# Optimization experiments

Measured on AMD Instinct MI355X. Metric: run time of the kernel, lower is better.

## Reference

```python
import jax, jax.numpy as jnp
from jax import lax
import numpy as np

D = 56      # latent_rep_size
H = 501     # GRU hidden size
T = 277     # repeat length (sequence length)
O = 76      # fc2 output


def setup_inputs() -> dict:
    key = jax.random.key(0)
    ks = jax.random.split(key, 20)
    B = 256
    s = 0.05
    inp = {"x": jax.random.normal(ks[0], (B, D), dtype=jnp.float32)}
    inp["fc1_w"] = jax.random.normal(ks[1], (D, D), dtype=jnp.float32) * s
    inp["fc1_b"] = jax.random.normal(ks[2], (D,), dtype=jnp.float32) * s
    k = 3
    for l, in_dim in enumerate([D, H, H]):
        inp[f"w_ih{l}"] = jax.random.normal(ks[k], (3 * H, in_dim), dtype=jnp.float32) * s; k += 1
        inp[f"w_hh{l}"] = jax.random.normal(ks[k], (3 * H, H), dtype=jnp.float32) * s; k += 1
        inp[f"b_ih{l}"] = jax.random.normal(ks[k], (3 * H,), dtype=jnp.float32) * s; k += 1
        inp[f"b_hh{l}"] = jax.random.normal(ks[k], (3 * H,), dtype=jnp.float32) * s; k += 1
    inp["fc2_w"] = jax.random.normal(ks[k], (O, H), dtype=jnp.float32) * s; k += 1
    inp["fc2_b"] = jax.random.normal(ks[k], (O,), dtype=jnp.float32) * s
    return inp


def _gru_step(h, g, w_hh, b_hh):
    # g: precomputed input gates (B, 3H) in PyTorch order [r, z, n]
    hg = h @ w_hh.T + b_hh                       # (B, 3H)
    r = jax.nn.sigmoid(g[:, :H] + hg[:, :H])
    z = jax.nn.sigmoid(g[:, H:2 * H] + hg[:, H:2 * H])
    n = jnp.tanh(g[:, 2 * H:] + r * hg[:, 2 * H:])
    h_new = (1.0 - z) * n + z * h
    return h_new, h_new


def _gru_layer(x_gates, w_hh, b_hh, B, dtype):
    # x_gates: (T, B, 3H) input contribution per timestep
    h0 = jnp.zeros((B, H), dtype)
    _, ys = lax.scan(lambda h, g: _gru_step(h, g, w_hh, b_hh), h0, x_gates)
    return ys  # (T, B, H)


def reference(x, fc1_w, fc1_b,
              w_ih0, w_hh0, b_ih0, b_hh0,
              w_ih1, w_hh1, b_ih1, b_hh1,
              w_ih2, w_hh2, b_ih2, b_hh2,
              fc2_w, fc2_b):
    B = x.shape[0]
    dtype = x.dtype
    # fc1 + relu, then the input is repeated 277 times -> layer-0 input gates
    # are identical at every timestep; compute them once (B, 3H).
    h_in = jax.nn.relu(x @ fc1_w.T + fc1_b)             # (B, D)
    g0 = h_in @ w_ih0.T + b_ih0                          # (B, 3H), constant over t
    h0 = jnp.zeros((B, H), dtype)
    _, ys0 = lax.scan(lambda h, _: _gru_step(h, g0, w_hh0, b_hh0), h0, None, length=T)
    # layers 1 and 2: precompute input gates for all timesteps, then scan
    g1 = jnp.einsum('tbh,gh->tbg', ys0, w_ih1) + b_ih1   # (T, B, 3H)
    ys1 = _gru_layer(g1, w_hh1, b_hh1, B, dtype)
    g2 = jnp.einsum('tbh,gh->tbg', ys1, w_ih2) + b_ih2
    ys2 = _gru_layer(g2, w_hh2, b_hh2, B, dtype)
    # fc2 then permute(1, 2, 0): (T, B, O) -> (B, O, T)
    out = jnp.einsum('tbh,oh->tbo', ys2, fc2_w) + fc2_b
    return jnp.transpose(out, (1, 2, 0))
```

## Files before the change

### kernel.cpp

```cpp
#include <hip/hip_runtime.h>
#include <hip/hip_bf16.h>
#include <math.h>

#define D_IN 56
#define H    501
#define T_STEPS 277
#define O_OUT 76
#define BATCH 256
#define HP   512
#define NP   1504
#define SSTR 520
#define HSTR 576

#define LDS_SA    0
#define LDS_SB    (32 * SSTR)
#define LDS_SC    (64 * SSTR)
#define LDS_STAGE (96 * SSTR)
#define DYN_LDS   (96 * SSTR * 2 + 18 * HSTR * 4 + 32 * 48 * 4 + 3 * 4 * 16 * 4)

typedef __attribute__((ext_vector_type(8))) short s16x8;
typedef __attribute__((ext_vector_type(4))) float f32x4;
typedef unsigned long long ull;

__device__ __forceinline__ short f2bf(float x) {
    union { float f; unsigned u; } v; v.f = x;
    unsigned r = (v.u + 0x7fffu + ((v.u >> 16) & 1u)) >> 16;
    return (short)r;
}
__device__ __forceinline__ float bf2f(short b) {
    union { unsigned u; float f; } v; v.u = ((unsigned)(unsigned short)b) << 16;
    return v.f;
}
__device__ __forceinline__ float sigm(float x) { return 1.f / (1.f + __expf(-x)); }
__device__ __forceinline__ float tanh_fast(float x) { return 1.f - 2.f / (1.f + __expf(2.f * x)); }

__device__ __forceinline__ void glds16(const void* g, void* l) {
    __builtin_amdgcn_global_load_lds((const __attribute__((address_space(1))) unsigned int*)g,
                                     (__attribute__((address_space(3))) unsigned int*)l,
                                     16, 0, 0);
}

__global__ void k_pack_gru(const float* __restrict__ w_ih,
                           const float* __restrict__ w_hh,
                           short* __restrict__ dst, int KT) {
    int tile = blockIdx.x;
    int ktp  = tile % KT;
    int g    = (tile / KT) % 3;
    int j    = tile / (KT * 3);
    int l    = threadIdx.x;
    int u    = j * 16 + (l & 15);
    int row  = g * H + u;
    const float* src; int k0;
    if (KT == 32) {
        if (ktp < 16) { src = w_ih; k0 = ktp * 32; }
        else          { src = w_hh; k0 = (ktp - 16) * 32; }
    } else          { src = w_hh; k0 = ktp * 32; }
    k0 += (l >> 4) * 8;
    short* p = dst + ((size_t)tile * 64 + l) * 8;
    for (int jj = 0; jj < 8; jj++) {
        int k = k0 + jj;
        float v = 0.f;
        if (u < H && k < H) v = src[(size_t)row * H + k];
        p[jj] = f2bf(v);
    }
}

__global__ void k_pack_fc2(const float* __restrict__ w, short* __restrict__ dst) {
    int tile = blockIdx.x;
    int kt = tile % 16, mt = tile / 16;
    int l = threadIdx.x;
    int o = mt * 16 + (l & 15);
    int k0 = kt * 32 + (l >> 4) * 8;
    short* p = dst + ((size_t)tile * 64 + l) * 8;
    for (int jj = 0; jj < 8; jj++) {
        int k = k0 + jj; float v = 0.f;
        if (o < O_OUT && k < H) v = w[(size_t)o * H + k];
        p[jj] = f2bf(v);
    }
}

__global__ void k_hin(const float* __restrict__ x, const float* __restrict__ w,
                      const float* __restrict__ bias, float* __restrict__ hin) {
    int b = blockIdx.x, o = threadIdx.x;
    float acc = 0.f;
    if (o < D_IN) {
        acc = bias[o];
        for (int k = 0; k < D_IN; k++) acc += x[b * D_IN + k] * w[o * D_IN + k];
        acc = fmaxf(acc, 0.f);
    }
    hin[b * 64 + o] = (o < D_IN) ? acc : 0.f;
}

__global__ void k_g0(const float* __restrict__ hin, const float* __restrict__ w_ih0,
                     const float* __restrict__ b_ih0, float* __restrict__ g0) {
    int b = blockIdx.x, tid = threadIdx.x;
    __shared__ float shx[D_IN];
    if (tid < D_IN) shx[tid] = hin[b * 64 + tid];
    __syncthreads();
    for (int o = tid; o < NP; o += 256) {
        float acc = 0.f;
        if (o < 3 * H) {
            acc = b_ih0[o];
            for (int k = 0; k < D_IN; k++) acc += shx[k] * w_ih0[(size_t)o * D_IN + k];
        }
        g0[(size_t)b * NP + o] = acc;
    }
}

template <int NK>
__device__ __forceinline__ void role_mfma_reg(const short* __restrict__ stg, int abase, int ak0,
                                              const s16x8 (&wv)[48],
                                              float* __restrict__ dr, float* __restrict__ dz,
                                              float* __restrict__ dn, int lane) {
    const int arow = lane & 15;
    const int acol = (lane >> 4) * 8;
    f32x4 ar0 = {0.f,0.f,0.f,0.f}, ar1 = {0.f,0.f,0.f,0.f};
    f32x4 az0 = {0.f,0.f,0.f,0.f}, az1 = {0.f,0.f,0.f,0.f};
    f32x4 an0 = {0.f,0.f,0.f,0.f}, an1 = {0.f,0.f,0.f,0.f};
    #pragma unroll
    for (int kk = 0; kk < NK; kk++) {
        int ak = ak0 + kk;
        s16x8 x0 = *(const s16x8*)&stg[abase + arow * SSTR + ak * 32 + acol];
        s16x8 x1 = *(const s16x8*)&stg[abase + (16 + arow) * SSTR + ak * 32 + acol];
        ar0 = __builtin_amdgcn_mfma_f32_16x16x32_bf16(x0, wv[3 * kk + 0], ar0, 0, 0, 0);
        ar1 = __builtin_amdgcn_mfma_f32_16x16x32_bf16(x1, wv[3 * kk + 0], ar1, 0, 0, 0);
        az0 = __builtin_amdgcn_mfma_f32_16x16x32_bf16(x0, wv[3 * kk + 1], az0, 0, 0, 0);
        az1 = __builtin_amdgcn_mfma_f32_16x16x32_bf16(x1, wv[3 * kk + 1], az1, 0, 0, 0);
        an0 = __builtin_amdgcn_mfma_f32_16x16x32_bf16(x0, wv[3 * kk + 2], an0, 0, 0, 0);
        an1 = __builtin_amdgcn_mfma_f32_16x16x32_bf16(x1, wv[3 * kk + 2], an1, 0, 0, 0);
    }
    int ul = lane & 15, mrow = (lane >> 4) * 4;
    #pragma unroll
    for (int r = 0; r < 4; r++) {
        dr[(mrow + r) * 18 + ul]      = ar0[r];
        dr[(16 + mrow + r) * 18 + ul] = ar1[r];
        dz[(mrow + r) * 18 + ul]      = az0[r];
        dz[(16 + mrow + r) * 18 + ul] = az1[r];
        dn[(mrow + r) * 18 + ul]      = an0[r];
        dn[(16 + mrow + r) * 18 + ul] = an1[r];
    }
}

__global__ __launch_bounds__(384, 2)
void k_gru_persist(const short* __restrict__ packW0,
                   const short* __restrict__ packW1,
                   const short* __restrict__ packW2,
                   const float* __restrict__ g0,
                   const float* __restrict__ b_hh0,
                   const float* __restrict__ b_ih1, const float* __restrict__ b_hh1,
                   const float* __restrict__ b_ih2, const float* __restrict__ b_hh2,
                   short* __restrict__ ysA,
                   short* __restrict__ ysB,
                   unsigned* __restrict__ cnt) {
    const int bg   = blockIdx.x & 7;
    const int j    = blockIdx.x >> 3;
    const int b0   = bg * 32;
    const int tid  = threadIdx.x;
    const int lane = tid & 63;
    const int wave = tid >> 6;
    const s16x8 z8 = {0, 0, 0, 0, 0, 0, 0, 0};

    extern __shared__ __align__(16) char smem[];
    short* stg = (short*)smem;
    float* hgl = (float*)(smem + LDS_STAGE * 2);
    float* sg0 = hgl + 18 * HSTR;
    float* sbb = sg0 + 32 * 48;

    int abase, ak0, slot0;
    s16x8 wv[48];
    {
        const short* wpk; int KT, kt0;
        switch (wave) {
            case 0:  wpk = packW0; KT = 16; kt0 = 0;  abase = LDS_SA; ak0 = 0; slot0 = 0;  break;
            case 1:  wpk = packW0; KT = 16; kt0 = 8;  abase = LDS_SA; ak0 = 8; slot0 = 1;  break;
            case 2:  wpk = packW1; KT = 32; kt0 = 0;  abase = LDS_SA; ak0 = 0; slot0 = 6;  break;
            case 3:  wpk = packW1; KT = 32; kt0 = 16; abase = LDS_SB; ak0 = 0; slot0 = 7;  break;
            case 4:  wpk = packW2; KT = 32; kt0 = 0;  abase = LDS_SB; ak0 = 0; slot0 = 12; break;
            default: wpk = packW2; KT = 32; kt0 = 16; abase = LDS_SC; ak0 = 0; slot0 = 13; break;
        }
        const volatile s16x8* vg0 = (const volatile s16x8*)(wpk + ((size_t)((j * 3 + 0) * KT + kt0) * 512));
        const volatile s16x8* vg1 = (const volatile s16x8*)(wpk + ((size_t)((j * 3 + 1) * KT + kt0) * 512));
        const volatile s16x8* vg2 = (const volatile s16x8*)(wpk + ((size_t)((j * 3 + 2) * KT + kt0) * 512));
        const int NKw = (wave < 2) ? 8 : 16;
        #pragma unroll
        for (int kk = 0; kk < 16; kk++) {
            if (kk < NKw) {
                wv[3 * kk + 0] = vg0[kk * 64 + lane];
                wv[3 * kk + 1] = vg1[kk * 64 + lane];
                wv[3 * kk + 2] = vg2[kk * 64 + lane];
            }
        }
    }
    float* dr = hgl + (size_t)slot0 * HSTR;
    float* dz = hgl + (size_t)(slot0 + 2) * HSTR;
    float* dn = hgl + (size_t)(slot0 + 4) * HSTR;

    for (int c = tid; c < 32 * 48; c += 384) {
        int m = c / 48, col = c % 48;
        int g = col >> 4, ul = col & 15;
        int u = j * 16 + ul;
        float v = 0.f;
        if (u < H) {
            v = g0[(size_t)(b0 + m) * NP + g * H + u];
            if (g == 0) v += b_hh0[u];
            else if (g == 1) v += b_hh0[H + u];
        }
        sg0[m * 48 + col] = v;
    }
    if (tid < 48) {
        int l = tid >> 4, ul = tid & 15, u = j * 16 + ul;
        float br = 0.f, bz = 0.f, bxn = 0.f, bhn = 0.f;
        if (u < H) {
            if (l == 0) bhn = b_hh0[2 * H + u];
            else {
                const float* bi = (l == 1) ? b_ih1 : b_ih2;
                const float* bh = (l == 1) ? b_hh1 : b_hh2;
                br = bi[u] + bh[u]; bz = bi[H + u] + bh[H + u];
                bxn = bi[2 * H + u]; bhn = bh[2 * H + u];
            }
        }
        sbb[(l * 4 + 0) * 16 + ul] = br;  sbb[(l * 4 + 1) * 16 + ul] = bz;
        sbb[(l * 4 + 2) * 16 + ul] = bxn; sbb[(l * 4 + 3) * 16 + ul] = bhn;
    }
    __syncthreads();

    unsigned* myflags = cnt + bg * 32;

    for (int s = 0; s < T_STEPS + 2; ++s) {
        const bool hasL0 = (s < T_STEPS);
        const bool hasL1 = (s >= 1 && s <= T_STEPS);
        const bool hasL2 = (s >= 2);
        const short* ysAm1 = ysA + (size_t)(s - 1) * BATCH * HP;
        const short* ysBm2 = ysB + (size_t)(s - 2) * BATCH * HP;
        const short* ysAm3 = ysA + (size_t)(s - 3) * BATCH * HP;

        {
            const bool needA = (s <= T_STEPS);
            const bool ldA   = (s >= 1) && needA;
            const bool needB = hasL1;
            const bool ldB   = (s >= 2) && needB;
            const bool needC = hasL2;
            const bool ldC   = (s >= 3);
            #pragma unroll
            for (int i = 0; i < 6; i++) {
                int r = wave + 6 * i;
                if (r < 32) {
                    size_t go = (size_t)(b0 + r) * HP + (size_t)lane * 8;
                    if (ldA)      glds16(ysAm1 + go, &stg[LDS_SA + r * SSTR]);
                    else if (needA) *(s16x8*)&stg[LDS_SA + r * SSTR + lane * 8] = z8;
                    if (ldB)      glds16(ysBm2 + go, &stg[LDS_SB + r * SSTR]);
                    else if (needB) *(s16x8*)&stg[LDS_SB + r * SSTR + lane * 8] = z8;
                    if (ldC) {
                        const ull* pc = (const ull*)(ysAm3 + go);
                        union { ull q[2]; s16x8 v; } uu;
                        uu.q[0] = __hip_atomic_load(pc,     __ATOMIC_RELAXED, __HIP_MEMORY_SCOPE_AGENT);
                        uu.q[1] = __hip_atomic_load(pc + 1, __ATOMIC_RELAXED, __HIP_MEMORY_SCOPE_AGENT);
                        *(s16x8*)&stg[LDS_SC + r * SSTR + lane * 8] = uu.v;
                    } else if (needC) {
                        *(s16x8*)&stg[LDS_SC + r * SSTR + lane * 8] = z8;
                    }
                }
            }
        }
        asm volatile("s_waitcnt vmcnt(0)" ::: "memory");
        __syncthreads();

        {
            const bool active = (wave < 2) ? hasL0 : ((wave < 4) ? hasL1 : hasL2);
            if (active) {
                if (wave < 2) role_mfma_reg<8>(stg, abase, ak0, wv, dr, dz, dn, lane);
                else          role_mfma_reg<16>(stg, abase, ak0, wv, dr, dz, dn, lane);
            }
        }
        __syncthreads();

        #pragma unroll
        for (int it = 0; it < 2; it++) {
            int idx = tid + it * 384;
            int which = idx >> 8, id8 = idx & 255;
            int m = id8 >> 3, pr = id8 & 7;
            int b = b0 + m;
            if (which == 0 && hasL0) {
                short* dst = ysA + (size_t)s * BATCH * HP;
                unsigned pk = 0;
                #pragma unroll
                for (int e = 0; e < 2; e++) {
                    int ul = pr * 2 + e, u = j * 16 + ul, mo = m * 18 + ul;
                    float hv = 0.f;
                    if (u < H) {
                        float hr = hgl[0 * HSTR + mo] + hgl[1 * HSTR + mo];
                        float hz = hgl[2 * HSTR + mo] + hgl[3 * HSTR + mo];
                        float hn = hgl[4 * HSTR + mo] + hgl[5 * HSTR + mo];
                        float r = sigm(sg0[m * 48 + ul] + hr);
                        float z = sigm(sg0[m * 48 + 16 + ul] + hz);
                        float n = tanh_fast(sg0[m * 48 + 32 + ul] + r * (hn + sbb[3 * 16 + ul]));
                        float hold = bf2f(stg[LDS_SA + m * SSTR + u]);
                        hv = (1.f - z) * n + z * hold;
                    }
                    pk |= ((unsigned)(unsigned short)f2bf(hv)) << (16 * e);
                }
                __hip_atomic_store((unsigned*)&dst[(size_t)b * HP + j * 16 + pr * 2], pk,
                                   __ATOMIC_RELAXED, __HIP_MEMORY_SCOPE_AGENT);
            } else if (which == 1 && hasL1) {
                short* dst = ysB + (size_t)(s - 1) * BATCH * HP;
                unsigned pk = 0;
                #pragma unroll
                for (int e = 0; e < 2; e++) {
                    int ul = pr * 2 + e, u = j * 16 + ul, mo = m * 18 + ul;
                    float hv = 0.f;
                    if (u < H) {
                        float xr = hgl[6 * HSTR + mo]  + sbb[(4 + 0) * 16 + ul];
                        float hr = hgl[7 * HSTR + mo];
                        float xz = hgl[8 * HSTR + mo]  + sbb[(4 + 1) * 16 + ul];
                        float hz = hgl[9 * HSTR + mo];
                        float xn = hgl[10 * HSTR + mo] + sbb[(4 + 2) * 16 + ul];
                        float hn = hgl[11 * HSTR + mo] + sbb[(4 + 3) * 16 + ul];
                        float r = sigm(xr + hr);
                        float z = sigm(xz + hz);
                        float n = tanh_fast(xn + r * hn);
                        float hold = bf2f(stg[LDS_SB + m * SSTR + u]);
                        hv = (1.f - z) * n + z * hold;
                    }
                    pk |= ((unsigned)(unsigned short)f2bf(hv)) << (16 * e);
                }
                __hip_atomic_store((unsigned*)&dst[(size_t)b * HP + j * 16 + pr * 2], pk,
                                   __ATOMIC_RELAXED, __HIP_MEMORY_SCOPE_AGENT);
            } else if (which == 2 && hasL2) {
                short* dst = ysA + (size_t)(s - 2) * BATCH * HP;
                unsigned pk = 0;
                #pragma unroll
                for (int e = 0; e < 2; e++) {
                    int ul = pr * 2 + e, u = j * 16 + ul, mo = m * 18 + ul;
                    float hv = 0.f;
                    if (u < H) {
                        float xr = hgl[12 * HSTR + mo] + sbb[(8 + 0) * 16 + ul];
                        float hr = hgl[13 * HSTR + mo];
                        float xz = hgl[14 * HSTR + mo] + sbb[(8 + 1) * 16 + ul];
                        float hz = hgl[15 * HSTR + mo];
                        float xn = hgl[16 * HSTR + mo] + sbb[(8 + 2) * 16 + ul];
                        float hn = hgl[17 * HSTR + mo] + sbb[(8 + 3) * 16 + ul];
                        float r = sigm(xr + hr);
                        float z = sigm(xz + hz);
                        float n = tanh_fast(xn + r * hn);
                        float hold = bf2f(stg[LDS_SC + m * SSTR + u]);
                        hv = (1.f - z) * n + z * hold;
                    }
                    pk |= ((unsigned)(unsigned short)f2bf(hv)) << (16 * e);
                }
                __hip_atomic_store((unsigned*)&dst[(size_t)b * HP + j * 16 + pr * 2], pk,
                                   __ATOMIC_RELAXED, __HIP_MEMORY_SCOPE_AGENT);
            }
        }
        __syncthreads();

        if (tid == 0) {
            asm volatile("s_waitcnt vmcnt(0)" ::: "memory");
            __hip_atomic_store(myflags + j, (unsigned)(s + 1),
                               __ATOMIC_RELAXED, __HIP_MEMORY_SCOPE_AGENT);
        }
        if (tid < 32) {
            const unsigned tgt = (unsigned)(s + 1);
            unsigned* fl = myflags + tid;
            for (;;) {
                unsigned v = __hip_atomic_load(fl, __ATOMIC_RELAXED, __HIP_MEMORY_SCOPE_AGENT);
                if (__all(v >= tgt)) break;
            }
        }
        __syncthreads();
    }
}

__global__ __launch_bounds__(256, 1)
void k_fc2(const short* __restrict__ ys2, const short* __restrict__ fc2p,
           const float* __restrict__ fc2_b, float* __restrict__ out) {
    int b = blockIdx.x;
    int tid = threadIdx.x, lane = tid & 63, wave = tid >> 6;
    const s16x8 zf = {0, 0, 0, 0, 0, 0, 0, 0};
    for (int ntile = wave; ntile < 18; ntile += 4) {
        int tt = ntile * 16 + (lane & 15);
        s16x8 bf[16];
        for (int kt = 0; kt < 16; kt++) {
            if (tt < T_STEPS)
                bf[kt] = *(const s16x8*)&ys2[((size_t)tt * BATCH + b) * HP + kt * 32 + (lane >> 4) * 8];
            else
                bf[kt] = zf;
        }
        for (int mt = 0; mt < 5; mt++) {
            f32x4 acc = {0.f, 0.f, 0.f, 0.f};
            for (int kt = 0; kt < 16; kt++) {
                s16x8 af = *(const s16x8*)&fc2p[(((size_t)mt * 16 + kt) * 64 + lane) * 8];
                acc = __builtin_amdgcn_mfma_f32_16x16x32_bf16(af, bf[kt], acc, 0, 0, 0);
            }
            int obase = mt * 16 + (lane >> 4) * 4;
            for (int r = 0; r < 4; r++) {
                int o = obase + r;
                if (o < O_OUT && tt < T_STEPS)
                    out[((size_t)b * O_OUT + o) * T_STEPS + tt] = acc[r] + fc2_b[o];
            }
        }
    }
}

extern "C" void kernel_launch(void* const* d_in, const int* in_sizes, int n_in,
                              void* d_out, int out_size, void* d_ws, size_t ws_size,
                              hipStream_t stream) {
    const float* x     = (const float*)d_in[0];
    const float* fc1_w = (const float*)d_in[1];
    const float* fc1_b = (const float*)d_in[2];
    const float* w_ih0 = (const float*)d_in[3];
    const float* w_hh0 = (const float*)d_in[4];
    const float* b_ih0 = (const float*)d_in[5];
    const float* b_hh0 = (const float*)d_in[6];
    const float* w_ih1 = (const float*)d_in[7];
    const float* w_hh1 = (const float*)d_in[8];
    const float* b_ih1 = (const float*)d_in[9];
    const float* b_hh1 = (const float*)d_in[10];
    const float* w_ih2 = (const float*)d_in[11];
    const float* w_hh2 = (const float*)d_in[12];
    const float* b_ih2 = (const float*)d_in[13];
    const float* b_hh2 = (const float*)d_in[14];
    const float* fc2_w = (const float*)d_in[15];
    const float* fc2_b = (const float*)d_in[16];
    float* out = (float*)d_out;

    char* p = (char*)d_ws;
    auto alloc = [&](size_t bytes) {
        char* r = p; p += (bytes + 255) & ~(size_t)255; return r;
    };
    short* packW0 = (short*)alloc((size_t)32 * 3 * 16 * 64 * 8 * 2);
    short* packW1 = (short*)alloc((size_t)32 * 3 * 32 * 64 * 8 * 2);
    short* packW2 = (short*)alloc((size_t)32 * 3 * 32 * 64 * 8 * 2);
    short* packF  = (short*)alloc((size_t)80 * 64 * 8 * 2);
    float* hin    = (float*)alloc((size_t)BATCH * 64 * 4);
    float* g0     = (float*)alloc((size_t)BATCH * NP * 4);
    unsigned* cnt = (unsigned*)alloc(256 * 4);
    short* ysA    = (short*)alloc((size_t)T_STEPS * BATCH * HP * 2);
    short* ysB    = (short*)alloc((size_t)T_STEPS * BATCH * HP * 2);

    static bool attr_set = false;
    if (!attr_set) {
        (void)hipFuncSetAttribute((const void*)k_gru_persist,
                                  hipFuncAttributeMaxDynamicSharedMemorySize,
                                  DYN_LDS);
        attr_set = true;
    }

    hipMemsetAsync(cnt, 0, 256 * 4, stream);
    k_pack_gru<<<32 * 3 * 16, 64, 0, stream>>>(nullptr, w_hh0, packW0, 16);
    k_pack_gru<<<32 * 3 * 32, 64, 0, stream>>>(w_ih1, w_hh1, packW1, 32);
    k_pack_gru<<<32 * 3 * 32, 64, 0, stream>>>(w_ih2, w_hh2, packW2, 32);
    k_pack_fc2<<<80, 64, 0, stream>>>(fc2_w, packF);
    k_hin<<<BATCH, 64, 0, stream>>>(x, fc1_w, fc1_b, hin);
    k_g0<<<BATCH, 256, 0, stream>>>(hin, w_ih0, b_ih0, g0);

    k_gru_persist<<<256, 384, DYN_LDS, stream>>>(packW0, packW1, packW2, g0,
                                                 b_hh0, b_ih1, b_hh1, b_ih2, b_hh2,
                                                 ysA, ysB, cnt);

    k_fc2<<<BATCH, 256, 0, stream>>>(ysA, packF, fc2_b, out);
}
```

Before: 2.468 ms.

## Rebalance GRU persistent kernel to 8 waves with LDS atomic-add accumulation

Grows the persistent GRU kernel from 6 to 8 waves per block and gives each wave an equal 10-tile share of the combined K work across all three layers. Segments may cross gate and layer boundaries, so partial results are summed with LDS atomicAdd into 15 accumulator slots instead of separate per-wave slots. The slots are zeroed by the gate-update threads after reading. The goal is to cut per-wave register pressure (30 weight vectors instead of 48) and remove the load imbalance where the layer-0 waves had half the work. The cost is LDS float atomics and extra zeroing stores on the serial per-step critical path.

```diff
diff --git a/kernel.cpp b/kernel.cpp
--- a/kernel.cpp
+++ b/kernel.cpp
@@ -11,12 +11,13 @@
 #define NP   1504
 #define SSTR 520
 #define HSTR 576
+#define NSLOT 15
 
 #define LDS_SA    0
 #define LDS_SB    (32 * SSTR)
 #define LDS_SC    (64 * SSTR)
 #define LDS_STAGE (96 * SSTR)
-#define DYN_LDS   (96 * SSTR * 2 + 18 * HSTR * 4 + 32 * 48 * 4 + 3 * 4 * 16 * 4)
+#define DYN_LDS   (96 * SSTR * 2 + NSLOT * HSTR * 4 + 32 * 48 * 4 + 3 * 4 * 16 * 4)
 
 typedef __attribute__((ext_vector_type(8))) short s16x8;
 typedef __attribute__((ext_vector_type(4))) float f32x4;
@@ -107,41 +108,51 @@
     }
 }
 
+template <int LEN>
+__device__ __forceinline__ void preload_w(s16x8* dst, const short* wpk, int KT,
+                                          int jj3, int ktA, int lane) {
+    #pragma unroll
+    for (int g = 0; g < 3; g++) {
+        const volatile s16x8* vp =
+            (const volatile s16x8*)(wpk + ((size_t)((jj3 + g) * KT + ktA) * 512));
+        #pragma unroll
+        for (int kk = 0; kk < LEN; kk++) dst[3 * kk + g] = vp[kk * 64 + lane];
+    }
+}
+
 template <int NK>
-__device__ __forceinline__ void role_mfma_reg(const short* __restrict__ stg, int abase, int ak0,
-                                              const s16x8 (&wv)[48],
-                                              float* __restrict__ dr, float* __restrict__ dz,
-                                              float* __restrict__ dn, int lane) {
+__device__ __forceinline__ void role_seg(const short* __restrict__ stg, int abase, int ak0,
+                                         const s16x8* __restrict__ wv,
+                                         float* __restrict__ hgl, int slotbase, int lane) {
     const int arow = lane & 15;
     const int acol = (lane >> 4) * 8;
-    f32x4 ar0 = {0.f,0.f,0.f,0.f}, ar1 = {0.f,0.f,0.f,0.f};
-    f32x4 az0 = {0.f,0.f,0.f,0.f}, az1 = {0.f,0.f,0.f,0.f};
-    f32x4 an0 = {0.f,0.f,0.f,0.f}, an1 = {0.f,0.f,0.f,0.f};
+    f32x4 a0[3], a1[3];
+    #pragma unroll
+    for (int g = 0; g < 3; g++) { a0[g] = (f32x4){0.f,0.f,0.f,0.f}; a1[g] = (f32x4){0.f,0.f,0.f,0.f}; }
     #pragma unroll
     for (int kk = 0; kk < NK; kk++) {
         int ak = ak0 + kk;
         s16x8 x0 = *(const s16x8*)&stg[abase + arow * SSTR + ak * 32 + acol];
         s16x8 x1 = *(const s16x8*)&stg[abase + (16 + arow) * SSTR + ak * 32 + acol];
-        ar0 = __builtin_amdgcn_mfma_f32_16x16x32_bf16(x0, wv[3 * kk + 0], ar0, 0, 0, 0);
-        ar1 = __builtin_amdgcn_mfma_f32_16x16x32_bf16(x1, wv[3 * kk + 0], ar1, 0, 0, 0);
-        az0 = __builtin_amdgcn_mfma_f32_16x16x32_bf16(x0, wv[3 * kk + 1], az0, 0, 0, 0);
-        az1 = __builtin_amdgcn_mfma_f32_16x16x32_bf16(x1, wv[3 * kk + 1], az1, 0, 0, 0);
-        an0 = __builtin_amdgcn_mfma_f32_16x16x32_bf16(x0, wv[3 * kk + 2], an0, 0, 0, 0);
-        an1 = __builtin_amdgcn_mfma_f32_16x16x32_bf16(x1, wv[3 * kk + 2], an1, 0, 0, 0);
-    }
-    int ul = lane & 15, mrow = (lane >> 4) * 4;
+        #pragma unroll
+        for (int g = 0; g < 3; g++) {
+            a0[g] = __builtin_amdgcn_mfma_f32_16x16x32_bf16(x0, wv[3 * kk + g], a0[g], 0, 0, 0);
+            a1[g] = __builtin_amdgcn_mfma_f32_16x16x32_bf16(x1, wv[3 * kk + g], a1[g], 0, 0, 0);
+        }
+    }
+    const int ul = lane & 15, mrow = (lane >> 4) * 4;
     #pragma unroll
-    for (int r = 0; r < 4; r++) {
-        dr[(mrow + r) * 18 + ul]      = ar0[r];
-        dr[(16 + mrow + r) * 18 + ul] = ar1[r];
-        dz[(mrow + r) * 18 + ul]      = az0[r];
-        dz[(16 + mrow + r) * 18 + ul] = az1[r];
-        dn[(mrow + r) * 18 + ul]      = an0[r];
-        dn[(16 + mrow + r) * 18 + ul] = an1[r];
-    }
-}
-
-__global__ __launch_bounds__(384, 2)
+    for (int g = 0; g < 3; g++) {
+        float* base = hgl + (size_t)(slotbase + g) * HSTR;
+        #pragma unroll
+        for (int r = 0; r < 4; r++) {
+            atomicAdd(&base[(mrow + r) * 18 + ul],      a0[g][r]);
+            atomicAdd(&base[(16 + mrow + r) * 18 + ul], a1[g][r]);
+        }
+    }
+}
+
+__global__ __launch_bounds__(512, 2)
 void k_gru_persist(const short* __restrict__ packW0,
                    const short* __restrict__ packW1,
                    const short* __restrict__ packW2,
@@ -163,39 +174,30 @@
     extern __shared__ __align__(16) char smem[];
     short* stg = (short*)smem;
     float* hgl = (float*)(smem + LDS_STAGE * 2);
-    float* sg0 = hgl + 18 * HSTR;
+    float* sg0 = hgl + NSLOT * HSTR;
     float* sbb = sg0 + 32 * 48;
 
-    int abase, ak0, slot0;
-    s16x8 wv[48];
+    s16x8 wv[30];
     {
-        const short* wpk; int KT, kt0;
+        const int jj3 = j * 3;
         switch (wave) {
-            case 0:  wpk = packW0; KT = 16; kt0 = 0;  abase = LDS_SA; ak0 = 0; slot0 = 0;  break;
-            case 1:  wpk = packW0; KT = 16; kt0 = 8;  abase = LDS_SA; ak0 = 8; slot0 = 1;  break;
-            case 2:  wpk = packW1; KT = 32; kt0 = 0;  abase = LDS_SA; ak0 = 0; slot0 = 6;  break;
-            case 3:  wpk = packW1; KT = 32; kt0 = 16; abase = LDS_SB; ak0 = 0; slot0 = 7;  break;
-            case 4:  wpk = packW2; KT = 32; kt0 = 0;  abase = LDS_SB; ak0 = 0; slot0 = 12; break;
-            default: wpk = packW2; KT = 32; kt0 = 16; abase = LDS_SC; ak0 = 0; slot0 = 13; break;
-        }
-        const volatile s16x8* vg0 = (const volatile s16x8*)(wpk + ((size_t)((j * 3 + 0) * KT + kt0) * 512));
-        const volatile s16x8* vg1 = (const volatile s16x8*)(wpk + ((size_t)((j * 3 + 1) * KT + kt0) * 512));
-        const volatile s16x8* vg2 = (const volatile s16x8*)(wpk + ((size_t)((j * 3 + 2) * KT + kt0) * 512));
-        const int NKw = (wave < 2) ? 8 : 16;
-        #pragma unroll
-        for (int kk = 0; kk < 16; kk++) {
-            if (kk < NKw) {
-                wv[3 * kk + 0] = vg0[kk * 64 + lane];
-                wv[3 * kk + 1] = vg1[kk * 64 + lane];
-                wv[3 * kk + 2] = vg2[kk * 64 + lane];
-            }
-        }
-    }
-    float* dr = hgl + (size_t)slot0 * HSTR;
-    float* dz = hgl + (size_t)(slot0 + 2) * HSTR;
-    float* dn = hgl + (size_t)(slot0 + 4) * HSTR;
-
-    for (int c = tid; c < 32 * 48; c += 384) {
+            case 0: preload_w<10>(wv,      packW0, 16, jj3, 0,      lane); break;
+            case 1: preload_w<6> (wv,      packW0, 16, jj3, 10,     lane);
+                    preload_w<4> (wv + 18, packW1, 32, jj3, 0,      lane); break;
+            case 2: preload_w<10>(wv,      packW1, 32, jj3, 4,      lane); break;
+            case 3: preload_w<2> (wv,      packW1, 32, jj3, 14,     lane);
+                    preload_w<8> (wv + 6,  packW1, 32, jj3, 16 + 0, lane); break;
+            case 4: preload_w<8> (wv,      packW1, 32, jj3, 16 + 8, lane);
+                    preload_w<2> (wv + 24, packW2, 32, jj3, 0,      lane); break;
+            case 5: preload_w<10>(wv,      packW2, 32, jj3, 2,      lane); break;
+            case 6: preload_w<4> (wv,      packW2, 32, jj3, 12,     lane);
+                    preload_w<6> (wv + 12, packW2, 32, jj3, 16 + 0, lane); break;
+            default: preload_w<10>(wv,     packW2, 32, jj3, 16 + 6, lane); break;
+        }
+    }
+
+    for (int c = tid; c < NSLOT * HSTR; c += 512) hgl[c] = 0.f;
+    for (int c = tid; c < 32 * 48; c += 512) {
         int m = c / 48, col = c % 48;
         int g = col >> 4, ul = col & 15;
         int u = j * 16 + ul;
@@ -237,46 +239,51 @@
         {
             const bool needA = (s <= T_STEPS);
             const bool ldA   = (s >= 1) && needA;
-            const bool needB = hasL1;
+            const bool needB = (s >= 1);
             const bool ldB   = (s >= 2) && needB;
             const bool needC = hasL2;
             const bool ldC   = (s >= 3);
             #pragma unroll
-            for (int i = 0; i < 6; i++) {
-                int r = wave + 6 * i;
-                if (r < 32) {
-                    size_t go = (size_t)(b0 + r) * HP + (size_t)lane * 8;
-                    if (ldA)      glds16(ysAm1 + go, &stg[LDS_SA + r * SSTR]);
-                    else if (needA) *(s16x8*)&stg[LDS_SA + r * SSTR + lane * 8] = z8;
-                    if (ldB)      glds16(ysBm2 + go, &stg[LDS_SB + r * SSTR]);
-                    else if (needB) *(s16x8*)&stg[LDS_SB + r * SSTR + lane * 8] = z8;
-                    if (ldC) {
-                        const ull* pc = (const ull*)(ysAm3 + go);
-                        union { ull q[2]; s16x8 v; } uu;
-                        uu.q[0] = __hip_atomic_load(pc,     __ATOMIC_RELAXED, __HIP_MEMORY_SCOPE_AGENT);
-                        uu.q[1] = __hip_atomic_load(pc + 1, __ATOMIC_RELAXED, __HIP_MEMORY_SCOPE_AGENT);
-                        *(s16x8*)&stg[LDS_SC + r * SSTR + lane * 8] = uu.v;
-                    } else if (needC) {
-                        *(s16x8*)&stg[LDS_SC + r * SSTR + lane * 8] = z8;
-                    }
+            for (int i = 0; i < 4; i++) {
+                int r = wave * 4 + i;
+                size_t go = (size_t)(b0 + r) * HP + (size_t)lane * 8;
+                if (ldA)        glds16(ysAm1 + go, &stg[LDS_SA + r * SSTR]);
+                else if (needA) *(s16x8*)&stg[LDS_SA + r * SSTR + lane * 8] = z8;
+                if (ldB)        glds16(ysBm2 + go, &stg[LDS_SB + r * SSTR]);
+                else if (needB) *(s16x8*)&stg[LDS_SB + r * SSTR + lane * 8] = z8;
+                if (ldC) {
+                    const ull* pc = (const ull*)(ysAm3 + go);
+                    union { ull q[2]; s16x8 v; } uu;
+                    uu.q[0] = __hip_atomic_load(pc,     __ATOMIC_RELAXED, __HIP_MEMORY_SCOPE_AGENT);
+                    uu.q[1] = __hip_atomic_load(pc + 1, __ATOMIC_RELAXED, __HIP_MEMORY_SCOPE_AGENT);
+                    *(s16x8*)&stg[LDS_SC + r * SSTR + lane * 8] = uu.v;
+                } else if (needC) {
+                    *(s16x8*)&stg[LDS_SC + r * SSTR + lane * 8] = z8;
                 }
             }
         }
         asm volatile("s_waitcnt vmcnt(0)" ::: "memory");
         __syncthreads();
 
-        {
-            const bool active = (wave < 2) ? hasL0 : ((wave < 4) ? hasL1 : hasL2);
-            if (active) {
-                if (wave < 2) role_mfma_reg<8>(stg, abase, ak0, wv, dr, dz, dn, lane);
-                else          role_mfma_reg<16>(stg, abase, ak0, wv, dr, dz, dn, lane);
-            }
+        switch (wave) {
+            case 0: if (hasL0) role_seg<10>(stg, LDS_SA, 0,  wv,      hgl, 0,  lane); break;
+            case 1: if (hasL0) role_seg<6> (stg, LDS_SA, 10, wv,      hgl, 0,  lane);
+                    if (hasL1) role_seg<4> (stg, LDS_SA, 0,  wv + 18, hgl, 3,  lane); break;
+            case 2: if (hasL1) role_seg<10>(stg, LDS_SA, 4,  wv,      hgl, 3,  lane); break;
+            case 3: if (hasL1) role_seg<2> (stg, LDS_SA, 14, wv,      hgl, 3,  lane);
+                    if (hasL1) role_seg<8> (stg, LDS_SB, 0,  wv + 6,  hgl, 6,  lane); break;
+            case 4: if (hasL1) role_seg<8> (stg, LDS_SB, 8,  wv,      hgl, 6,  lane);
+                    if (hasL2) role_seg<2> (stg, LDS_SB, 0,  wv + 24, hgl, 9,  lane); break;
+            case 5: if (hasL2) role_seg<10>(stg, LDS_SB, 2,  wv,      hgl, 9,  lane); break;
+            case 6: if (hasL2) role_seg<4> (stg, LDS_SB, 12, wv,      hgl, 9,  lane);
+                    if (hasL2) role_seg<6> (stg, LDS_SC, 0,  wv + 12, hgl, 12, lane); break;
+            default: if (hasL2) role_seg<10>(stg, LDS_SC, 6, wv,      hgl, 12, lane); break;
         }
         __syncthreads();
 
         #pragma unroll
         for (int it = 0; it < 2; it++) {
-            int idx = tid + it * 384;
+            int idx = tid + it * 512;
             int which = idx >> 8, id8 = idx & 255;
             int m = id8 >> 3, pr = id8 & 7;
             int b = b0 + m;
@@ -288,9 +295,10 @@
                     int ul = pr * 2 + e, u = j * 16 + ul, mo = m * 18 + ul;
                     float hv = 0.f;
                     if (u < H) {
-                        float hr = hgl[0 * HSTR + mo] + hgl[1 * HSTR + mo];
-                        float hz = hgl[2 * HSTR + mo] + hgl[3 * HSTR + mo];
-                        float hn = hgl[4 * HSTR + mo] + hgl[5 * HSTR + mo];
+                        float hr = hgl[0 * HSTR + mo];
+                        float hz = hgl[1 * HSTR + mo];
+                        float hn = hgl[2 * HSTR + mo];
+                        hgl[0 * HSTR + mo] = 0.f; hgl[1 * HSTR + mo] = 0.f; hgl[2 * HSTR + mo] = 0.f;
                         float r = sigm(sg0[m * 48 + ul] + hr);
                         float z = sigm(sg0[m * 48 + 16 + ul] + hz);
                         float n = tanh_fast(sg0[m * 48 + 32 + ul] + r * (hn + sbb[3 * 16 + ul]));
@@ -309,12 +317,14 @@
                     int ul = pr * 2 + e, u = j * 16 + ul, mo = m * 18 + ul;
                     float hv = 0.f;
                     if (u < H) {
-                        float xr = hgl[6 * HSTR + mo]  + sbb[(4 + 0) * 16 + ul];
-                        float hr = hgl[7 * HSTR + mo];
-                        float xz = hgl[8 * HSTR + mo]  + sbb[(4 + 1) * 16 + ul];
-                        float hz = hgl[9 * HSTR + mo];
-                        float xn = hgl[10 * HSTR + mo] + sbb[(4 + 2) * 16 + ul];
-                        float hn = hgl[11 * HSTR + mo] + sbb[(4 + 3) * 16 + ul];
+                        float xr = hgl[3 * HSTR + mo] + sbb[(4 + 0) * 16 + ul];
+                        float xz = hgl[4 * HSTR + mo] + sbb[(4 + 1) * 16 + ul];
+                        float xn = hgl[5 * HSTR + mo] + sbb[(4 + 2) * 16 + ul];
+                        float hr = hgl[6 * HSTR + mo];
+                        float hz = hgl[7 * HSTR + mo];
+                        float hn = hgl[8 * HSTR + mo] + sbb[(4 + 3) * 16 + ul];
+                        hgl[3 * HSTR + mo] = 0.f; hgl[4 * HSTR + mo] = 0.f; hgl[5 * HSTR + mo] = 0.f;
+                        hgl[6 * HSTR + mo] = 0.f; hgl[7 * HSTR + mo] = 0.f; hgl[8 * HSTR + mo] = 0.f;
                         float r = sigm(xr + hr);
                         float z = sigm(xz + hz);
                         float n = tanh_fast(xn + r * hn);
@@ -333,12 +343,14 @@
                     int ul = pr * 2 + e, u = j * 16 + ul, mo = m * 18 + ul;
                     float hv = 0.f;
                     if (u < H) {
-                        float xr = hgl[12 * HSTR + mo] + sbb[(8 + 0) * 16 + ul];
-                        float hr = hgl[13 * HSTR + mo];
-                        float xz = hgl[14 * HSTR + mo] + sbb[(8 + 1) * 16 + ul];
-                        float hz = hgl[15 * HSTR + mo];
-                        float xn = hgl[16 * HSTR + mo] + sbb[(8 + 2) * 16 + ul];
-                        float hn = hgl[17 * HSTR + mo] + sbb[(8 + 3) * 16 + ul];
+                        float xr = hgl[9  * HSTR + mo] + sbb[(8 + 0) * 16 + ul];
+                        float xz = hgl[10 * HSTR + mo] + sbb[(8 + 1) * 16 + ul];
+                        float xn = hgl[11 * HSTR + mo] + sbb[(8 + 2) * 16 + ul];
+                        float hr = hgl[12 * HSTR + mo];
+                        float hz = hgl[13 * HSTR + mo];
+                        float hn = hgl[14 * HSTR + mo] + sbb[(8 + 3) * 16 + ul];
+                        hgl[9  * HSTR + mo] = 0.f; hgl[10 * HSTR + mo] = 0.f; hgl[11 * HSTR + mo] = 0.f;
+                        hgl[12 * HSTR + mo] = 0.f; hgl[13 * HSTR + mo] = 0.f; hgl[14 * HSTR + mo] = 0.f;
                         float r = sigm(xr + hr);
                         float z = sigm(xz + hz);
                         float n = tanh_fast(xn + r * hn);
@@ -453,7 +465,7 @@
     k_hin<<<BATCH, 64, 0, stream>>>(x, fc1_w, fc1_b, hin);
     k_g0<<<BATCH, 256, 0, stream>>>(hin, w_ih0, b_ih0, g0);
 
-    k_gru_persist<<<256, 384, DYN_LDS, stream>>>(packW0, packW1, packW2, g0,
+    k_gru_persist<<<256, 512, DYN_LDS, stream>>>(packW0, packW1, packW2, g0,
                                                  b_hh0, b_ih1, b_hh1, b_ih2, b_hh2,
                                                  ysA, ysB, cnt);
 
```

After: 8.301 ms. 236% more time.
